# Optimization experiments

Measured on AMD Instinct MI355X. Metric: run time of the kernel, lower is better.

The kernel has to match this reference:

```python
import jax, jax.numpy as jnp
import numpy as np
import math

NEG_INF = -1e38


def wkv_scan(w, u, k, v):
    """Numerically-stable RWKV WKV recurrence.
    w, u: [C] (w is already -exp(time_decay)); k, v: [B, T, C] -> y: [B, T, C]."""
    B, T, C = k.shape

    def step(carry, kv_t):
        a, b, pp = carry            # running num/den in log-max form, [B, C]
        kt, vt = kv_t               # [B, C]
        ww = u + kt
        q = jnp.maximum(pp, ww)
        e1 = jnp.exp(pp - q)
        e2 = jnp.exp(ww - q)
        y = (e1 * a + e2 * vt) / (e1 * b + e2)
        # state update with decay w
        ww2 = pp + w
        q2 = jnp.maximum(ww2, kt)
        e1b = jnp.exp(ww2 - q2)
        e2b = jnp.exp(kt - q2)
        return (e1b * a + e2b * vt, e1b * b + e2b, q2), y

    init = (jnp.zeros((B, C), k.dtype), jnp.zeros((B, C), k.dtype),
            jnp.full((B, C), NEG_INF, k.dtype))
    kT = jnp.swapaxes(k, 0, 1)      # [T, B, C]
    vT = jnp.swapaxes(v, 0, 1)
    _, ys = jax.lax.scan(step, init, (kT, vT))
    return jnp.swapaxes(ys, 0, 1)   # [B, T, C]


def setup_inputs() -> dict:
    key = jax.random.key(0)
    B, T, C = 16, 1024, 1024
    k1, k2, k3, k4 = jax.random.split(key, 4)
    x = jax.random.normal(k1, (B, T, C), dtype=jnp.float32)
    scale = 0.02
    Wk = jax.random.normal(k2, (C, C), dtype=jnp.float32) * scale
    Wr = jax.random.normal(k3, (C, C), dtype=jnp.float32) * scale
    Wo = jax.random.normal(k4, (C, C), dtype=jnp.float32) * scale
    # faithful parameter init from RWKVTimeMix.__init__
    h = np.arange(C, dtype=np.float64)
    decay_speed = -5.0 + 8.0 * (h / (C - 1)) ** (0.7 + 1.3 * 1)
    zigzag = (((np.arange(C) + 1) % 3) - 1) * 0.5
    time_first = np.ones(C) * math.log(0.3) + zigzag
    return {
        "x": x,
        "Wk": Wk,
        "Wr": Wr,
        "Wo": Wo,
        "time_decay": jnp.asarray(decay_speed, dtype=jnp.float32),
        "time_first": jnp.asarray(time_first, dtype=jnp.float32),
    }


def reference(x, Wk, Wr, Wo, time_decay, time_first):
    # k = key(x); r = receptance(x); NOTE: source uses receptance for v as well
    k = jnp.einsum('btc,hc->bth', x, Wk)
    r = jnp.einsum('btc,hc->bth', x, Wr)
    v = r  # faithful to source: v = self.receptance(input)
    w = -jnp.exp(time_decay)
    y = wkv_scan(w, time_first, k, v)
    out = jax.nn.sigmoid(r) * y
    return jnp.einsum('bth,ch->btc', out, Wo)
```

## Files before the change

### kernel.cpp

```cpp
#include <hip/hip_runtime.h>
#include <hip/hip_bf16.h>


typedef __attribute__((ext_vector_type(8))) short bf16x8;
typedef __attribute__((ext_vector_type(4))) float f32x4;
typedef unsigned short u16;

#define GK   1024
#define NKT  16
#define ROWB 2048l

#define NCH  16384
#define NC   16
#define CL   64

__device__ __forceinline__ void async_copy16(const void* g, void* l) {
    __builtin_amdgcn_global_load_lds(
        (const __attribute__((address_space(1))) void*)g,
        (__attribute__((address_space(3))) void*)l,
        16 , 0 , 0 );
}

__global__ __launch_bounds__(256) void cast_all_kernel(
    const float* __restrict__ x,  const float* __restrict__ wk,
    const float* __restrict__ wr, const float* __restrict__ wo,
    __hip_bfloat16* __restrict__ xb,  __hip_bfloat16* __restrict__ wkb,
    __hip_bfloat16* __restrict__ wrb, __hip_bfloat16* __restrict__ wob)
{
    const int bid = blockIdx.x;
    const float* src;
    __hip_bfloat16* dst;
    int blk;
    if (bid < 16384)      { src = x;  dst = xb;  blk = bid; }
    else if (bid < 17408) { src = wk; dst = wkb; blk = bid - 16384; }
    else if (bid < 18432) { src = wr; dst = wrb; blk = bid - 17408; }
    else                  { src = wo; dst = wob; blk = bid - 18432; }

    const int i = blk * 1024 + threadIdx.x * 4;
    const f32x4 v = *(const f32x4*)(src + i);
    __hip_bfloat16 o[4];
    o[0] = __float2bfloat16(v[0]);
    o[1] = __float2bfloat16(v[1]);
    o[2] = __float2bfloat16(v[2]);
    o[3] = __float2bfloat16(v[3]);
    *(__attribute__((ext_vector_type(4))) short*)(dst + i) =
        *(__attribute__((ext_vector_type(4))) short*)o;
}


#define PHASE(I0, STAGE_STMT) do {                                            \
    bf16x8 a00 = *(const bf16x8*)(As + arow + (I0) * 2048 + ck0);             \
    bf16x8 a01 = *(const bf16x8*)(As + arow + (I0) * 2048 + ck1);             \
    bf16x8 a10 = *(const bf16x8*)(As + arow + (I0 + 1) * 2048 + ck0);         \
    bf16x8 a11 = *(const bf16x8*)(As + arow + (I0 + 1) * 2048 + ck1);         \
    STAGE_STMT;                                                               \
    __builtin_amdgcn_s_barrier();                                             \
    asm volatile("s_waitcnt lgkmcnt(0)" ::: "memory");                        \
    __builtin_amdgcn_sched_barrier(0);                                        \
    __builtin_amdgcn_s_setprio(1);                                            \
    _Pragma("unroll")                                                         \
    for (int n = 0; n < 4; ++n) {                                             \
        acc[I0][n]     = __builtin_amdgcn_mfma_f32_16x16x32_bf16(             \
                             a00, bf[n][0], acc[I0][n], 0, 0, 0);             \
        acc[I0][n]     = __builtin_amdgcn_mfma_f32_16x16x32_bf16(             \
                             a01, bf[n][1], acc[I0][n], 0, 0, 0);             \
        acc[I0 + 1][n] = __builtin_amdgcn_mfma_f32_16x16x32_bf16(             \
                             a10, bf[n][0], acc[I0 + 1][n], 0, 0, 0);         \
        acc[I0 + 1][n] = __builtin_amdgcn_mfma_f32_16x16x32_bf16(             \
                             a11, bf[n][1], acc[I0 + 1][n], 0, 0, 0);         \
    }                                                                         \
    __builtin_amdgcn_s_setprio(0);                                            \
    __builtin_amdgcn_s_barrier();                                            \
} while (0)

template <typename OutT>
__global__ __launch_bounds__(512, 2) void gemm256_kernel(
    const __hip_bfloat16* __restrict__ A,
    const __hip_bfloat16* __restrict__ B0,
    const __hip_bfloat16* __restrict__ B1,
    OutT* __restrict__ C,
    int ldc, int nsplit, int ntn)
{
    __shared__ __align__(16) char lds[131072];

    const int tid = threadIdx.x;

    const int nwg = gridDim.x;
    const int cpx = nwg >> 3;
    const int wg  = blockIdx.x;
    const int swz = (wg & 7) * cpx + (wg >> 3);
    const int bm  = (swz / ntn) * 256;
    const int bn  = (swz % ntn) * 256;

    const __hip_bfloat16* Bsrc;
    int bnl;
    if (bn < nsplit) { Bsrc = B0; bnl = bn; }
    else             { Bsrc = B1; bnl = bn - nsplit; }

    const int lane = tid & 63;
    const int wave = tid >> 6;
    const int nl   = lane & 15;
    const int quad = lane >> 4;
    const int wm   = (wave >> 2) * 128;
    const int wn   = (wave & 3) * 64;

    const int r0 = tid >> 3;
    const int cs = ((tid & 7) ^ (r0 & 7)) << 4;
    const int od = tid * 16;
    const char* Ag = (const char*)A    + (size_t)(bm  + r0) * ROWB + cs;
    const char* Bg = (const char*)Bsrc + (size_t)(bnl + r0) * ROWB + cs;

    char* ldsA0 = lds;
    char* ldsB0 = lds + 32768;
    char* ldsA1 = lds + 65536;
    char* ldsB1 = lds + 98304;

    auto stageA = [&](int kt, int h, char* dstA) {
        const char* g = Ag + (size_t)h * 128 * ROWB + (size_t)kt * 128;
        async_copy16(g,             dstA + h * 16384 + od);
        async_copy16(g + 64 * ROWB, dstA + h * 16384 + od + 8192);
    };
    auto stageB = [&](int kt, int h, char* dstB) {
        const char* g = Bg + (size_t)h * 128 * ROWB + (size_t)kt * 128;
        async_copy16(g,             dstB + h * 16384 + od);
        async_copy16(g + 64 * ROWB, dstB + h * 16384 + od + 8192);
    };

    const int rw   = nl & 7;
    const int ck0  = (quad ^ rw) << 4;
    const int ck1  = ((4 + quad) ^ rw) << 4;
    const int arow = (wm + nl) * 128;
    const int brow = (wn + nl) * 128;

    f32x4 acc[8][4] = {};

    stageB(0, 0, ldsB0); stageB(0, 1, ldsB0);
    stageA(0, 0, ldsA0); stageA(0, 1, ldsA0);
    stageB(1, 0, ldsB1); stageB(1, 1, ldsB1);
    asm volatile("s_waitcnt vmcnt(4)" ::: "memory");
    __builtin_amdgcn_s_barrier();

#pragma unroll 2
    for (int t = 0; t < NKT; ++t) {
        char* As = (t & 1) ? ldsA1 : ldsA0;
        char* Bs = (t & 1) ? ldsB1 : ldsB0;
        char* Ao = (t & 1) ? ldsA0 : ldsA1;

        bf16x8 bf[4][2];
#pragma unroll
        for (int n = 0; n < 4; ++n) {
            bf[n][0] = *(const bf16x8*)(Bs + brow + n * 2048 + ck0);
            bf[n][1] = *(const bf16x8*)(Bs + brow + n * 2048 + ck1);
        }

        PHASE(0, if (t + 1 < NKT) stageA(t + 1, 0, Ao));
        PHASE(2, if (t + 1 < NKT) stageA(t + 1, 1, Ao));
        PHASE(4, if (t + 2 < NKT) stageB(t + 2, 0, Bs));
        PHASE(6, {
            if (t + 2 < NKT) {
                stageB(t + 2, 1, Bs);
                asm volatile("s_waitcnt vmcnt(4)" ::: "memory");
            } else {
                asm volatile("s_waitcnt vmcnt(0)" ::: "memory");
            }
        });
    }

#pragma unroll
    for (int i = 0; i < 8; ++i) {
#pragma unroll
        for (int n = 0; n < 4; ++n) {
            const int col = bn + wn + n * 16 + nl;
#pragma unroll
            for (int r = 0; r < 4; ++r) {
                const int m = bm + wm + i * 16 + quad * 4 + r;
                const float vv = acc[i][n][r];
                if constexpr (__is_same(OutT, float))
                    C[(size_t)m * ldc + col] = vv;
                else
                    C[(size_t)m * ldc + col] = __float2bfloat16(vv);
            }
        }
    }
}

#define L2E 1.4426950408889634f

struct Blk { u16 k[8]; u16 v[8]; };

__device__ __forceinline__ void load8(const u16* kp, const u16* vp,
                                      int t, int S, Blk& B) {
#pragma unroll
    for (int j = 0; j < 8; ++j) {
        B.k[j] = kp[(size_t)(t + j) * S];
        B.v[j] = vp[(size_t)(t + j) * S];
    }
}

__device__ __forceinline__ float bf2f(u16 r) {
    return __uint_as_float(((unsigned)r) << 16);
}

__device__ __forceinline__ void wkv_state_step(
    u16 kraw, u16 vraw, float w2, float& a, float& bb, float& pp2)
{
    const float kf = bf2f(kraw);
    const float vf = bf2f(vraw);
    const float k2 = kf * L2E;
    const float d   = pp2 + w2 - k2;
    const float m0  = fminf(d, 0.f);
    const float e1b = __builtin_amdgcn_exp2f(m0);
    const float e2b = __builtin_amdgcn_exp2f(m0 - d);
    a   = e1b * a  + e2b * vf;
    bb  = e1b * bb + e2b;
    pp2 = k2 + fmaxf(d, 0.f);
}

__device__ __forceinline__ void wkv_step(
    u16 kraw, u16 vraw, float u2, float w2,
    float& a, float& bb, float& pp2, __hip_bfloat16* op)
{
    const float kf = bf2f(kraw);
    const float vf = bf2f(vraw);
    const float k2 = kf * L2E;

    const float ww2 = u2 + k2;
    const float s   = __builtin_amdgcn_exp2f(fminf(pp2 - ww2, 60.f));
    const float num = s * a + vf;
    const float den = s * bb + 1.f;
    const float e   = __builtin_amdgcn_exp2f(-L2E * vf);
    const float res = num * __builtin_amdgcn_rcpf(den * (1.f + e));
    *op = __float2bfloat16(res);

    const float d   = pp2 + w2 - k2;
    const float m0  = fminf(d, 0.f);
    const float e1b = __builtin_amdgcn_exp2f(m0);
    const float e2b = __builtin_amdgcn_exp2f(m0 - d);
    a   = e1b * a  + e2b * vf;
    bb  = e1b * bb + e2b;
    pp2 = k2 + fmaxf(d, 0.f);
}

__global__ __launch_bounds__(256) void wkv_agg_kernel(
    const __hip_bfloat16* __restrict__ kr,
    const float* __restrict__ td,
    float* __restrict__ aggA, float* __restrict__ aggB,
    float* __restrict__ aggP, int T, int C)
{
    const int gid2  = blockIdx.x * 256 + threadIdx.x;
    const int ch    = gid2 & (NCH - 1);
    const int chunk = gid2 >> 14;
    const int b = ch >> 10;
    const int c = ch & (C - 1);
    const int S = 2 * C;

    const float w2 = -__expf(td[c]) * L2E;

    const u16* kp = (const u16*)(kr + (size_t)b * T * S + c)
                    + (size_t)(chunk * CL) * S;
    const u16* vp = kp + C;

    float a = 0.f, bb = 0.f, pp2 = -1.4427e38f;

    Blk A, Bq;
    load8(kp, vp, 0, S, A);
    for (int tb = 0; tb < CL; tb += 16) {
        load8(kp, vp, tb + 8, S, Bq);
#pragma unroll
        for (int j = 0; j < 8; ++j)
            wkv_state_step(A.k[j], A.v[j], w2, a, bb, pp2);
        if (tb + 16 < CL) load8(kp, vp, tb + 16, S, A);
#pragma unroll
        for (int j = 0; j < 8; ++j)
            wkv_state_step(Bq.k[j], Bq.v[j], w2, a, bb, pp2);
    }
    aggA[gid2] = a;
    aggB[gid2] = bb;
    aggP[gid2] = pp2;
}

__global__ __launch_bounds__(256) void wkv_out_kernel(
    const __hip_bfloat16* __restrict__ kr,
    const float* __restrict__ tf, const float* __restrict__ td,
    const float* __restrict__ aggA, const float* __restrict__ aggB,
    const float* __restrict__ aggP,
    __hip_bfloat16* __restrict__ sy, int T, int C)
{
    const int gid2  = blockIdx.x * 256 + threadIdx.x;
    const int ch    = gid2 & (NCH - 1);
    const int chunk = gid2 >> 14;
    const int b = ch >> 10;
    const int c = ch & (C - 1);
    const int S = 2 * C;

    const float u2 = tf[c] * L2E;
    const float w2 = -__expf(td[c]) * L2E;

    float a = 0.f, bb = 0.f, pp2 = -1.4427e38f;
    for (int j = 0; j < chunk; ++j) {
        const float p  = aggP[j * NCH + ch]
                         + (float)((chunk - 1 - j) * CL) * w2;
        const float Aj = aggA[j * NCH + ch];
        const float Bj = aggB[j * NCH + ch];
        const float q  = fmaxf(pp2, p);
        const float e1 = __builtin_amdgcn_exp2f(pp2 - q);
        const float e2 = __builtin_amdgcn_exp2f(p - q);
        a   = e1 * a  + e2 * Aj;
        bb  = e1 * bb + e2 * Bj;
        pp2 = q;
    }

    const int t0 = chunk * CL;
    const u16* kp = (const u16*)(kr + (size_t)b * T * S + c) + (size_t)t0 * S;
    const u16* vp = kp + C;
    __hip_bfloat16* op = sy + (size_t)b * T * C + (size_t)t0 * C + c;

    Blk A, Bq;
    load8(kp, vp, 0, S, A);
    for (int tb = 0; tb < CL; tb += 16) {
        load8(kp, vp, tb + 8, S, Bq);
#pragma unroll
        for (int j = 0; j < 8; ++j)
            wkv_step(A.k[j], A.v[j], u2, w2, a, bb, pp2,
                     op + (size_t)(tb + j) * C);
        if (tb + 16 < CL) load8(kp, vp, tb + 16, S, A);
#pragma unroll
        for (int j = 0; j < 8; ++j)
            wkv_step(Bq.k[j], Bq.v[j], u2, w2, a, bb, pp2,
                     op + (size_t)(tb + 8 + j) * C);
    }
}

extern "C" void kernel_launch(void* const* d_in, const int* in_sizes, int n_in,
                              void* d_out, int out_size, void* d_ws, size_t ws_size,
                              hipStream_t stream) {
    const float* x  = (const float*)d_in[0];
    const float* Wk = (const float*)d_in[1];
    const float* Wr = (const float*)d_in[2];
    const float* Wo = (const float*)d_in[3];
    const float* td = (const float*)d_in[4];
    const float* tf = (const float*)d_in[5];
    float* out = (float*)d_out;

    const int B = 16, T = 1024, C = 1024;
    const int M = B * T;
    const int MC = M * C;
    const int CC = C * C;

    __hip_bfloat16* xb  = (__hip_bfloat16*)d_ws;
    __hip_bfloat16* Wkb = xb + (size_t)MC;
    __hip_bfloat16* Wrb = Wkb + (size_t)CC;
    __hip_bfloat16* Wob = Wrb + (size_t)CC;
    __hip_bfloat16* sy  = xb;

    float* aggA = (float*)Wkb;
    float* aggB = aggA + (size_t)NCH * NC;
    float* aggP = (float*)Wrb;

    __hip_bfloat16* kr = (__hip_bfloat16*)d_out;

    cast_all_kernel<<<dim3(16384 + 3 * 1024), 256, 0, stream>>>(
        x, Wk, Wr, Wo, xb, Wkb, Wrb, Wob);

    gemm256_kernel<__hip_bfloat16><<<dim3((M / 256) * (2 * C / 256)), 512, 0,
                                     stream>>>(xb, Wkb, Wrb, kr, 2 * C, C, 8);

    wkv_agg_kernel<<<dim3(NCH * NC / 256), 256, 0, stream>>>(
        kr, td, aggA, aggB, aggP, T, C);

    wkv_out_kernel<<<dim3(NCH * NC / 256), 256, 0, stream>>>(
        kr, tf, td, aggA, aggB, aggP, sy, T, C);

    gemm256_kernel<float><<<dim3((M / 256) * (C / 256)), 512, 0, stream>>>(
        sy, Wob, Wob, out, C, C, 4);
}
```

Baseline: 257.4 us.

## Store k/r projection transposed so WKV scans read time-contiguous vectors

The first GEMM now writes its bf16 output transposed (channel-major, time-contiguous), packing four consecutive rows into one 8-byte store. The WKV aggregate and output kernels then read k and v as 16-byte vectors along time instead of strided 2-byte scalar loads. This is meant to cut the number of memory transactions in the scan kernels. In exchange, each scan thread now reads its own contiguous stretch, so adjacent lanes no longer share cache lines, and the GEMM epilogue stores are strided by M.

```diff
diff --git a/kernel.cpp b/kernel.cpp
--- a/kernel.cpp
+++ b/kernel.cpp
@@ -4,6 +4,7 @@
 
 typedef __attribute__((ext_vector_type(8))) short bf16x8;
 typedef __attribute__((ext_vector_type(4))) float f32x4;
+typedef __attribute__((ext_vector_type(4))) short s16x4;
 typedef unsigned short u16;
 
 #define GK   1024
@@ -13,6 +14,7 @@
 #define NCH  16384
 #define NC   16
 #define CL   64
+#define MTOT 16384
 
 __device__ __forceinline__ void async_copy16(const void* g, void* l) {
     __builtin_amdgcn_global_load_lds(
@@ -43,8 +45,7 @@
     o[1] = __float2bfloat16(v[1]);
     o[2] = __float2bfloat16(v[2]);
     o[3] = __float2bfloat16(v[3]);
-    *(__attribute__((ext_vector_type(4))) short*)(dst + i) =
-        *(__attribute__((ext_vector_type(4))) short*)o;
+    *(s16x4*)(dst + i) = *(s16x4*)o;
 }
 
 
@@ -73,7 +74,7 @@
     __builtin_amdgcn_s_barrier();                                            \
 } while (0)
 
-template <typename OutT>
+template <typename OutT, bool TR>
 __global__ __launch_bounds__(512, 2) void gemm256_kernel(
     const __hip_bfloat16* __restrict__ A,
     const __hip_bfloat16* __restrict__ B0,
@@ -171,31 +172,29 @@
 #pragma unroll
         for (int n = 0; n < 4; ++n) {
             const int col = bn + wn + n * 16 + nl;
-#pragma unroll
-            for (int r = 0; r < 4; ++r) {
-                const int m = bm + wm + i * 16 + quad * 4 + r;
-                const float vv = acc[i][n][r];
-                if constexpr (__is_same(OutT, float))
-                    C[(size_t)m * ldc + col] = vv;
-                else
-                    C[(size_t)m * ldc + col] = __float2bfloat16(vv);
+            if constexpr (TR) {
+                const int m0 = bm + wm + i * 16 + quad * 4;
+                __hip_bfloat16 o[4];
+#pragma unroll
+                for (int r = 0; r < 4; ++r)
+                    o[r] = __float2bfloat16(acc[i][n][r]);
+                *(s16x4*)((u16*)C + (size_t)col * ldc + m0) = *(s16x4*)o;
+            } else {
+#pragma unroll
+                for (int r = 0; r < 4; ++r) {
+                    const int m = bm + wm + i * 16 + quad * 4 + r;
+                    const float vv = acc[i][n][r];
+                    if constexpr (__is_same(OutT, float))
+                        C[(size_t)m * ldc + col] = vv;
+                    else
+                        C[(size_t)m * ldc + col] = __float2bfloat16(vv);
+                }
             }
         }
     }
 }
 
 #define L2E 1.4426950408889634f
-
-struct Blk { u16 k[8]; u16 v[8]; };
-
-__device__ __forceinline__ void load8(const u16* kp, const u16* vp,
-                                      int t, int S, Blk& B) {
-#pragma unroll
-    for (int j = 0; j < 8; ++j) {
-        B.k[j] = kp[(size_t)(t + j) * S];
-        B.v[j] = vp[(size_t)(t + j) * S];
-    }
-}
 
 __device__ __forceinline__ float bf2f(u16 r) {
     return __uint_as_float(((unsigned)r) << 16);
@@ -242,7 +241,7 @@
 }
 
 __global__ __launch_bounds__(256) void wkv_agg_kernel(
-    const __hip_bfloat16* __restrict__ kr,
+    const __hip_bfloat16* __restrict__ krT,
     const float* __restrict__ td,
     float* __restrict__ aggA, float* __restrict__ aggB,
     float* __restrict__ aggP, int T, int C)
@@ -252,27 +251,29 @@
     const int chunk = gid2 >> 14;
     const int b = ch >> 10;
     const int c = ch & (C - 1);
-    const int S = 2 * C;
 
     const float w2 = -__expf(td[c]) * L2E;
 
-    const u16* kp = (const u16*)(kr + (size_t)b * T * S + c)
-                    + (size_t)(chunk * CL) * S;
-    const u16* vp = kp + C;
+    const u16* kp = (const u16*)krT + (size_t)c * MTOT + b * T + chunk * CL;
+    const u16* vp = (const u16*)krT + (size_t)(C + c) * MTOT + b * T
+                    + chunk * CL;
 
     float a = 0.f, bb = 0.f, pp2 = -1.4427e38f;
 
-    Blk A, Bq;
-    load8(kp, vp, 0, S, A);
+    bf16x8 ka = *(const bf16x8*)kp, va = *(const bf16x8*)vp, kb, vb;
     for (int tb = 0; tb < CL; tb += 16) {
-        load8(kp, vp, tb + 8, S, Bq);
+        kb = *(const bf16x8*)(kp + tb + 8);
+        vb = *(const bf16x8*)(vp + tb + 8);
 #pragma unroll
         for (int j = 0; j < 8; ++j)
-            wkv_state_step(A.k[j], A.v[j], w2, a, bb, pp2);
-        if (tb + 16 < CL) load8(kp, vp, tb + 16, S, A);
+            wkv_state_step((u16)ka[j], (u16)va[j], w2, a, bb, pp2);
+        if (tb + 16 < CL) {
+            ka = *(const bf16x8*)(kp + tb + 16);
+            va = *(const bf16x8*)(vp + tb + 16);
+        }
 #pragma unroll
         for (int j = 0; j < 8; ++j)
-            wkv_state_step(Bq.k[j], Bq.v[j], w2, a, bb, pp2);
+            wkv_state_step((u16)kb[j], (u16)vb[j], w2, a, bb, pp2);
     }
     aggA[gid2] = a;
     aggB[gid2] = bb;
@@ -280,7 +281,7 @@
 }
 
 __global__ __launch_bounds__(256) void wkv_out_kernel(
-    const __hip_bfloat16* __restrict__ kr,
+    const __hip_bfloat16* __restrict__ krT,
     const float* __restrict__ tf, const float* __restrict__ td,
     const float* __restrict__ aggA, const float* __restrict__ aggB,
     const float* __restrict__ aggP,
@@ -291,7 +292,6 @@
     const int chunk = gid2 >> 14;
     const int b = ch >> 10;
     const int c = ch & (C - 1);
-    const int S = 2 * C;
 
     const float u2 = tf[c] * L2E;
     const float w2 = -__expf(td[c]) * L2E;
@@ -311,22 +311,25 @@
     }
 
     const int t0 = chunk * CL;
-    const u16* kp = (const u16*)(kr + (size_t)b * T * S + c) + (size_t)t0 * S;
-    const u16* vp = kp + C;
+    const u16* kp = (const u16*)krT + (size_t)c * MTOT + b * T + t0;
+    const u16* vp = (const u16*)krT + (size_t)(C + c) * MTOT + b * T + t0;
     __hip_bfloat16* op = sy + (size_t)b * T * C + (size_t)t0 * C + c;
 
-    Blk A, Bq;
-    load8(kp, vp, 0, S, A);
+    bf16x8 ka = *(const bf16x8*)kp, va = *(const bf16x8*)vp, kb, vb;
     for (int tb = 0; tb < CL; tb += 16) {
-        load8(kp, vp, tb + 8, S, Bq);
+        kb = *(const bf16x8*)(kp + tb + 8);
+        vb = *(const bf16x8*)(vp + tb + 8);
 #pragma unroll
         for (int j = 0; j < 8; ++j)
-            wkv_step(A.k[j], A.v[j], u2, w2, a, bb, pp2,
+            wkv_step((u16)ka[j], (u16)va[j], u2, w2, a, bb, pp2,
                      op + (size_t)(tb + j) * C);
-        if (tb + 16 < CL) load8(kp, vp, tb + 16, S, A);
+        if (tb + 16 < CL) {
+            ka = *(const bf16x8*)(kp + tb + 16);
+            va = *(const bf16x8*)(vp + tb + 16);
+        }
 #pragma unroll
         for (int j = 0; j < 8; ++j)
-            wkv_step(Bq.k[j], Bq.v[j], u2, w2, a, bb, pp2,
+            wkv_step((u16)kb[j], (u16)vb[j], u2, w2, a, bb, pp2,
                      op + (size_t)(tb + 8 + j) * C);
     }
 }
@@ -357,20 +360,21 @@
     float* aggB = aggA + (size_t)NCH * NC;
     float* aggP = (float*)Wrb;
 
-    __hip_bfloat16* kr = (__hip_bfloat16*)d_out;
+    __hip_bfloat16* krT = (__hip_bfloat16*)d_out;
 
     cast_all_kernel<<<dim3(16384 + 3 * 1024), 256, 0, stream>>>(
         x, Wk, Wr, Wo, xb, Wkb, Wrb, Wob);
 
-    gemm256_kernel<__hip_bfloat16><<<dim3((M / 256) * (2 * C / 256)), 512, 0,
-                                     stream>>>(xb, Wkb, Wrb, kr, 2 * C, C, 8);
+    gemm256_kernel<__hip_bfloat16, true>
+        <<<dim3((M / 256) * (2 * C / 256)), 512, 0, stream>>>(
+            xb, Wkb, Wrb, krT, M, C, 8);
 
     wkv_agg_kernel<<<dim3(NCH * NC / 256), 256, 0, stream>>>(
-        kr, td, aggA, aggB, aggP, T, C);
+        krT, td, aggA, aggB, aggP, T, C);
 
     wkv_out_kernel<<<dim3(NCH * NC / 256), 256, 0, stream>>>(
-        kr, tf, td, aggA, aggB, aggP, sy, T, C);
-
-    gemm256_kernel<float><<<dim3((M / 256) * (C / 256)), 512, 0, stream>>>(
-        sy, Wob, Wob, out, C, C, 4);
-}
+        krT, tf, td, aggA, aggB, aggP, sy, T, C);
+
+    gemm256_kernel<float, false><<<dim3((M / 256) * (C / 256)), 512, 0,
+                                   stream>>>(sy, Wob, Wob, out, C, C, 4);
+}
```

Result: slower. 309.6 us (+20.3%).
